# Kernel optimization log

Measured on AMD Instinct MI355X. Metric: run time of the kernel, lower is better.

The kernel has to match this reference:

```python
import jax, jax.numpy as jnp
import numpy as np

IN_DIM, H1, H2, N_CLASSES = 128, 100, 128, 19
BATCH, SEQ = 512, 256


def _lstm_relu(x, W, U, b, units):
    """Keras LSTM with activation='relu', recurrent_activation='sigmoid'.
    x: [B, T, D]. Returns (all hidden states [B, T, units], last hidden [B, units]).
    Gate order (Keras): i, f, g(cell candidate), o.
    """
    B = x.shape[0]
    h0 = jnp.zeros((B, units), x.dtype)
    c0 = jnp.zeros((B, units), x.dtype)

    # precompute input projections for all timesteps: [T, B, 4*units]
    zx = jnp.einsum('btd,dk->tbk', x, W) + b

    def step(carry, zx_t):
        h, c = carry
        z = zx_t + h @ U
        i, f, g, o = jnp.split(z, 4, axis=-1)
        i = jax.nn.sigmoid(i)
        f = jax.nn.sigmoid(f)
        g = jax.nn.relu(g)          # activation='relu'
        o = jax.nn.sigmoid(o)
        c = f * c + i * g
        h = o * jax.nn.relu(c)      # output activation is also relu
        return (h, c), h

    (h_last, _), hs = jax.lax.scan(step, (h0, c0), zx)
    return jnp.transpose(hs, (1, 0, 2)), h_last


def setup_inputs() -> dict:
    key = jax.random.key(0)
    ks = jax.random.split(key, 9)
    def w(k, shape, fan_in):
        return jax.random.normal(k, shape, jnp.float32) / np.sqrt(fan_in)
    x = jax.random.normal(ks[0], (BATCH, SEQ, IN_DIM), jnp.float32)
    return {
        'x': x,
        'W1': w(ks[1], (IN_DIM, 4 * H1), IN_DIM),
        'U1': w(ks[2], (H1, 4 * H1), H1),
        'b1': jnp.zeros((4 * H1,), jnp.float32),
        'W2': w(ks[3], (H1, 4 * H2), H1),
        'U2': w(ks[4], (H2, 4 * H2), H2),
        'b2': jnp.zeros((4 * H2,), jnp.float32),
        'Wd': w(ks[5], (H2, N_CLASSES), H2),
        'bd': jnp.zeros((N_CLASSES,), jnp.float32),
    }


def reference(x, W1, U1, b1, W2, U2, b2, Wd, bd):
    h1_seq, _ = _lstm_relu(x, W1, U1, b1, H1)      # [B, T, 100]
    _, h2 = _lstm_relu(h1_seq, W2, U2, b2, H2)     # [B, 128] (last step only)
    logits = h2 @ Wd + bd
    return jax.nn.softmax(logits, axis=-1)         # [B, 19]
```

## Files before the change

kernel.cpp:

```cpp
#include <hip/hip_runtime.h>
#include <math.h>


#define T_SEQ 256
#define BATCH 512
#define IN_DIM 128
#define H1 100
#define H2 128
#define NCLS 19

typedef float f4v __attribute__((ext_vector_type(4)));

__device__ __forceinline__ float sigmoidf_(float x) {
    return 1.0f / (1.0f + __expf(-x));
}
__device__ __forceinline__ float hsum4_(f4v v) {
    return (v.x + v.y) + (v.z + v.w);
}

#define REP7(M)  M(0) M(1) M(2) M(3) M(4) M(5) M(6)
#define REP8(M)  M(0) M(1) M(2) M(3) M(4) M(5) M(6) M(7)

template<int K, int N, bool SWAP>
__global__ __launch_bounds__(256, 2)
void proj_kernel(const float* __restrict__ A, const float* __restrict__ W,
                 const float* __restrict__ bias, float* __restrict__ out)
{
    constexpr int LD = 132;
    __shared__ __align__(16) float As[32 * LD];
    __shared__ __align__(16) float Ws[32 * LD];
    const int tid = threadIdx.x;
    const int r0 = blockIdx.x * 128;
    const int c0 = blockIdx.y * 128;
    const int ty = tid >> 4, tx = tid & 15;

#define PACC(i) f4v accL##i = {0.f,0.f,0.f,0.f}; f4v accR##i = {0.f,0.f,0.f,0.f};
    REP8(PACC)
#undef PACC

    for (int kk = 0; kk < K; kk += 32) {
        __syncthreads();
#pragma unroll
        for (int i = 0; i < 4; ++i) {
            int idx = tid + i * 256;
            int row = idx >> 3, kg = idx & 7;
            int k = kk + kg * 4;
            f4v v = {0.f, 0.f, 0.f, 0.f};
            if (k < K) v = *(const f4v*)&A[(size_t)(r0 + row) * K + k];
            As[(kg * 4 + 0) * LD + row] = v.x;
            As[(kg * 4 + 1) * LD + row] = v.y;
            As[(kg * 4 + 2) * LD + row] = v.z;
            As[(kg * 4 + 3) * LD + row] = v.w;
        }
#pragma unroll
        for (int i = 0; i < 4; ++i) {
            int idx = tid + i * 256;
            int k = idx >> 5, cg = idx & 31;
            int gk = kk + k, gc = c0 + cg * 4;
            f4v v = {0.f, 0.f, 0.f, 0.f};
            if (gk < K && gc < N) v = *(const f4v*)&W[(size_t)gk * N + gc];
            *(f4v*)&Ws[k * LD + cg * 4] = v;
        }
        __syncthreads();
#pragma unroll
        for (int k = 0; k < 32; ++k) {
            f4v av0 = *(const f4v*)&As[k * LD + ty * 8];
            f4v av1 = *(const f4v*)&As[k * LD + ty * 8 + 4];
            f4v b0v = *(const f4v*)&Ws[k * LD + tx * 8];
            f4v b1v = *(const f4v*)&Ws[k * LD + tx * 8 + 4];
#define PFMA(i, s) accL##i += (s) * b0v; accR##i += (s) * b1v;
            PFMA(0, av0.x) PFMA(1, av0.y) PFMA(2, av0.z) PFMA(3, av0.w)
            PFMA(4, av1.x) PFMA(5, av1.y) PFMA(6, av1.z) PFMA(7, av1.w)
#undef PFMA
        }
    }

    const int cb = c0 + tx * 8;
    float b0 = (cb + 0 < N) ? bias[cb + 0] : 0.f;
    float b1 = (cb + 1 < N) ? bias[cb + 1] : 0.f;
    float b2 = (cb + 2 < N) ? bias[cb + 2] : 0.f;
    float b3 = (cb + 3 < N) ? bias[cb + 3] : 0.f;
    float b4 = (cb + 4 < N) ? bias[cb + 4] : 0.f;
    float b5 = (cb + 5 < N) ? bias[cb + 5] : 0.f;
    float b6 = (cb + 6 < N) ? bias[cb + 6] : 0.f;
    float b7 = (cb + 7 < N) ? bias[cb + 7] : 0.f;
    f4v bL = {b0, b1, b2, b3};
    f4v bR = {b4, b5, b6, b7};
#define PST(i) { \
        int r = r0 + ty * 8 + i; \
        size_t orow = SWAP ? ((size_t)(r & 255) * BATCH + (r >> 8)) : (size_t)r; \
        if (cb < N)     { f4v v = accL##i + bL; *(f4v*)&out[orow * N + cb] = v; } \
        if (cb + 4 < N) { f4v v = accR##i + bR; *(f4v*)&out[orow * N + cb + 4] = v; } }
    REP8(PST)
#undef PST
}

__device__ __forceinline__ f4v ldw_(const float* __restrict__ U1, int kb, int col) {
    f4v v;
    v.x = (kb + 0 < H1) ? U1[(size_t)(kb + 0) * 400 + col] : 0.f;
    v.y = (kb + 1 < H1) ? U1[(size_t)(kb + 1) * 400 + col] : 0.f;
    v.z = (kb + 2 < H1) ? U1[(size_t)(kb + 2) * 400 + col] : 0.f;
    v.w = (kb + 3 < H1) ? U1[(size_t)(kb + 3) * 400 + col] : 0.f;
    return v;
}

__global__ __launch_bounds__(512)
__attribute__((amdgpu_waves_per_eu(2, 2)))
void rec1_kernel(const float* __restrict__ zx,
                 const float* __restrict__ U1,
                 float* __restrict__ h1seq)
{
    const int row = blockIdx.x;
    const int tid = threadIdx.x;
    const int kq = tid >> 7;
    const int cl = tid & 127;
    const int cc = (cl < H1) ? cl : 0;
    __shared__ __align__(16) float hsP[112];
    __shared__ __align__(16) float zp[4][4][128];

#define R1W(j) \
    f4v w0_##j = ldw_(U1, kq * 28 + 4 * (j), cc); \
    f4v w1_##j = ldw_(U1, kq * 28 + 4 * (j), 100 + cc); \
    f4v w2_##j = ldw_(U1, kq * 28 + 4 * (j), 200 + cc); \
    f4v w3_##j = ldw_(U1, kq * 28 + 4 * (j), 300 + cc);
    REP7(R1W)
#undef R1W

    if (tid < 112) hsP[tid] = 0.0f;
    const bool tail = (kq == 0) && (cl < H1);
    float cst = 0.0f;
    float zc0 = 0.f, zc1 = 0.f, zc2 = 0.f, zc3 = 0.f;
    if (tail) {
        const float* pz = zx + (size_t)row * 400 + cl;
        zc0 = pz[0]; zc1 = pz[100]; zc2 = pz[200]; zc3 = pz[300];
    }
    __syncthreads();

    for (int t = 0; t < T_SEQ; ++t) {
        f4v s0 = {0.f, 0.f, 0.f, 0.f};
        f4v s1 = {0.f, 0.f, 0.f, 0.f};
        f4v s2 = {0.f, 0.f, 0.f, 0.f};
        f4v s3 = {0.f, 0.f, 0.f, 0.f};
#define R1F(j) { f4v hv = *(const f4v*)&hsP[kq * 28 + 4 * (j)]; \
        s0 += hv * w0_##j; s1 += hv * w1_##j; s2 += hv * w2_##j; s3 += hv * w3_##j; }
        REP7(R1F)
#undef R1F
        zp[kq][0][cl] = hsum4_(s0);
        zp[kq][1][cl] = hsum4_(s1);
        zp[kq][2][cl] = hsum4_(s2);
        zp[kq][3][cl] = hsum4_(s3);
        __syncthreads();

        if (tail) {
            int tn = (t + 1 < T_SEQ) ? t + 1 : t;
            const float* pz = zx + ((size_t)tn * BATCH + row) * 400 + cl;
            float zn0 = pz[0], zn1 = pz[100], zn2 = pz[200], zn3 = pz[300];

            float z0 = zc0 + ((zp[0][0][cl] + zp[1][0][cl]) + (zp[2][0][cl] + zp[3][0][cl]));
            float z1 = zc1 + ((zp[0][1][cl] + zp[1][1][cl]) + (zp[2][1][cl] + zp[3][1][cl]));
            float z2 = zc2 + ((zp[0][2][cl] + zp[1][2][cl]) + (zp[2][2][cl] + zp[3][2][cl]));
            float z3 = zc3 + ((zp[0][3][cl] + zp[1][3][cl]) + (zp[2][3][cl] + zp[3][3][cl]));
            float iv = sigmoidf_(z0);
            float fv = sigmoidf_(z1);
            float gv = fmaxf(z2, 0.0f);
            float ov = sigmoidf_(z3);
            cst = fv * cst + iv * gv;
            float h = ov * fmaxf(cst, 0.0f);
            hsP[cl] = h;
            h1seq[((size_t)t * BATCH + row) * H1 + cl] = h;
            zc0 = zn0; zc1 = zn1; zc2 = zn2; zc3 = zn3;
        }
        __syncthreads();
    }
}

template<bool INIT, bool LAST>
__global__ __launch_bounds__(512)
__attribute__((amdgpu_waves_per_eu(2, 2)))
void rec2_chunk(const float* __restrict__ zx,
                const float* __restrict__ U2,
                float* __restrict__ cbuf,
                float* __restrict__ hbuf,
                float* __restrict__ h2out,
                int tlen)
{
    const int row = blockIdx.x;
    const int tid = threadIdx.x;
    const int kq = tid >> 7;
    const int cl = tid & 127;
    __shared__ __align__(16) float hs[H2];
    __shared__ float zp[4 * 512];
    __shared__ float za[512];

#define R2_LD(j) \
    f4v w0_##j, w1_##j, w2_##j, w3_##j; { \
        const float* p = U2 + (size_t)(kq * 32 + 4 * j) * 512 + cl; \
        w0_##j = (f4v){p[0],   p[512],       p[1024],       p[1536]}; \
        w1_##j = (f4v){p[128], p[512 + 128], p[1024 + 128], p[1536 + 128]}; \
        w2_##j = (f4v){p[256], p[512 + 256], p[1024 + 256], p[1536 + 256]}; \
        w3_##j = (f4v){p[384], p[512 + 384], p[1024 + 384], p[1536 + 384]}; }
    REP8(R2_LD)
#undef R2_LD

    float cst = 0.0f;
    if (tid < H2) {
        if (INIT) {
            hs[tid] = 0.0f;
        } else {
            hs[tid] = hbuf[(size_t)row * H2 + tid];
            cst = cbuf[(size_t)row * H2 + tid];
        }
    }
    float zc = zx[(size_t)row * 512 + tid];
    __syncthreads();

    for (int t = 0; t < tlen; ++t) {
        int tn = (t + 1 < tlen) ? t + 1 : t;
        float zn = zx[((size_t)tn * BATCH + row) * 512 + tid];

        f4v s0 = {0.f, 0.f, 0.f, 0.f};
        f4v s1 = {0.f, 0.f, 0.f, 0.f};
        f4v s2 = {0.f, 0.f, 0.f, 0.f};
        f4v s3 = {0.f, 0.f, 0.f, 0.f};
#define R2_FMA(j) { f4v hv = *(const f4v*)&hs[kq * 32 + 4 * j]; \
        s0 += hv * w0_##j; s1 += hv * w1_##j; s2 += hv * w2_##j; s3 += hv * w3_##j; }
        REP8(R2_FMA)
#undef R2_FMA
        zp[kq * 512 + cl]       = hsum4_(s0);
        zp[kq * 512 + cl + 128] = hsum4_(s1);
        zp[kq * 512 + cl + 256] = hsum4_(s2);
        zp[kq * 512 + cl + 384] = hsum4_(s3);
        __syncthreads();

        float z = zc + (zp[tid] + zp[512 + tid]) + (zp[1024 + tid] + zp[1536 + tid]);
        float a = (tid >= 2 * H2 && tid < 3 * H2) ? fmaxf(z, 0.0f) : sigmoidf_(z);
        za[tid] = a;
        __syncthreads();

        if (tid < H2) {
            float i = za[tid], f = za[tid + 128], g = za[tid + 256], o = za[tid + 384];
            cst = f * cst + i * g;
            hs[tid] = o * fmaxf(cst, 0.0f);
        }
        __syncthreads();
        zc = zn;
    }

    if (tid < H2) {
        float h = hs[tid];
        cbuf[(size_t)row * H2 + tid] = cst;
        hbuf[(size_t)row * H2 + tid] = h;
        if (LAST) h2out[(size_t)row * H2 + tid] = h;
    }
}

__global__ __launch_bounds__(64, 1)
void dense_softmax_kernel(const float* __restrict__ h2, const float* __restrict__ Wd,
                          const float* __restrict__ bd, float* __restrict__ out)
{
    const int b = blockIdx.x;
    const int k = threadIdx.x;
    __shared__ __align__(16) float hsm[H2];
    if (k < H2 / 4) ((f4v*)hsm)[k] = ((const f4v*)(h2 + (size_t)b * H2))[k];
    __syncthreads();

    float logit = -1e30f;
    if (k < NCLS) {
        float acc = bd[k];
#pragma unroll
        for (int d = 0; d < H2; ++d) acc += hsm[d] * Wd[d * NCLS + k];
        logit = acc;
    }
    float m = logit;
#pragma unroll
    for (int off = 32; off >= 1; off >>= 1) m = fmaxf(m, __shfl_xor(m, off, 64));
    float e = (k < NCLS) ? __expf(logit - m) : 0.0f;
    float s = e;
#pragma unroll
    for (int off = 32; off >= 1; off >>= 1) s += __shfl_xor(s, off, 64);
    if (k < NCLS) out[(size_t)b * NCLS + k] = e / s;
}

__global__ __launch_bounds__(448, 1)
void lstm1_fb(const float* __restrict__ x, const float* __restrict__ W1,
              const float* __restrict__ U1, const float* __restrict__ b1,
              float* __restrict__ h1out)
{
    const int b = blockIdx.x;
    const int k = threadIdx.x;
    __shared__ __align__(16) float xs[IN_DIM];
    __shared__ __align__(16) float hs[H1];
    __shared__ __align__(16) float zs[4 * H1];
    float w1r[IN_DIM];
    float u1r[H1];
    float bias = 0.0f;
    if (k < 4 * H1) {
        bias = b1[k];
#pragma unroll
        for (int d = 0; d < IN_DIM; ++d) w1r[d] = W1[d * (4 * H1) + k];
#pragma unroll
        for (int j = 0; j < H1; ++j) u1r[j] = U1[j * (4 * H1) + k];
    }
    if (k < H1) hs[k] = 0.0f;
    if (k < IN_DIM / 4)
        ((float4*)xs)[k] = ((const float4*)(x + ((size_t)b * T_SEQ) * IN_DIM))[k];
    float c = 0.0f;
    __syncthreads();
    for (int t = 0; t < T_SEQ; ++t) {
        if (k < 4 * H1) {
            float acc0 = bias, acc1 = 0.f, acc2 = 0.f, acc3 = 0.f;
#pragma unroll
            for (int q = 0; q < IN_DIM / 4; ++q) {
                float4 xv = ((const float4*)xs)[q];
                acc0 += xv.x * w1r[4 * q]; acc1 += xv.y * w1r[4 * q + 1];
                acc2 += xv.z * w1r[4 * q + 2]; acc3 += xv.w * w1r[4 * q + 3];
            }
#pragma unroll
            for (int q = 0; q < H1 / 4; ++q) {
                float4 hv = ((const float4*)hs)[q];
                acc0 += hv.x * u1r[4 * q]; acc1 += hv.y * u1r[4 * q + 1];
                acc2 += hv.z * u1r[4 * q + 2]; acc3 += hv.w * u1r[4 * q + 3];
            }
            float zv = (acc0 + acc1) + (acc2 + acc3);
            zs[k] = (k >= 2 * H1 && k < 3 * H1) ? fmaxf(zv, 0.0f) : sigmoidf_(zv);
        }
        __syncthreads();
        if (k < H1) {
            float i = zs[k], f = zs[k + H1], g = zs[k + 2 * H1], o = zs[k + 3 * H1];
            c = f * c + i * g;
            float h = o * fmaxf(c, 0.0f);
            hs[k] = h;
            h1out[((size_t)t * BATCH + b) * H1 + k] = h;
        }
        int tn = t + 1;
        if (tn < T_SEQ && k < IN_DIM / 4)
            ((float4*)xs)[k] = ((const float4*)(x + ((size_t)b * T_SEQ + tn) * IN_DIM))[k];
        __syncthreads();
    }
}

__global__ __launch_bounds__(512, 1)
void lstm2_fb(const float* __restrict__ h1in, const float* __restrict__ W2,
              const float* __restrict__ U2, const float* __restrict__ b2,
              float* __restrict__ h2out)
{
    const int b = blockIdx.x;
    const int k = threadIdx.x;
    __shared__ __align__(16) float ps[H1];
    __shared__ __align__(16) float hs[H2];
    __shared__ __align__(16) float zs[4 * H2];
    float w2r[H1];
    float u2r[H2];
    float bias = b2[k];
#pragma unroll
    for (int j = 0; j < H1; ++j) w2r[j] = W2[j * (4 * H2) + k];
#pragma unroll
    for (int j = 0; j < H2; ++j) u2r[j] = U2[j * (4 * H2) + k];
    if (k < H2) hs[k] = 0.0f;
    if (k < H1 / 4)
        ((float4*)ps)[k] = ((const float4*)(h1in + (size_t)b * H1))[k];
    float c = 0.0f;
    float hlast = 0.0f;
    __syncthreads();
    for (int t = 0; t < T_SEQ; ++t) {
        float acc0 = bias, acc1 = 0.f, acc2 = 0.f, acc3 = 0.f;
#pragma unroll
        for (int q = 0; q < H1 / 4; ++q) {
            float4 pv = ((const float4*)ps)[q];
            acc0 += pv.x * w2r[4 * q]; acc1 += pv.y * w2r[4 * q + 1];
            acc2 += pv.z * w2r[4 * q + 2]; acc3 += pv.w * w2r[4 * q + 3];
        }
#pragma unroll
        for (int q = 0; q < H2 / 4; ++q) {
            float4 hv = ((const float4*)hs)[q];
            acc0 += hv.x * u2r[4 * q]; acc1 += hv.y * u2r[4 * q + 1];
            acc2 += hv.z * u2r[4 * q + 2]; acc3 += hv.w * u2r[4 * q + 3];
        }
        float zv = (acc0 + acc1) + (acc2 + acc3);
        zs[k] = (k >= 2 * H2 && k < 3 * H2) ? fmaxf(zv, 0.0f) : sigmoidf_(zv);
        __syncthreads();
        if (k < H2) {
            float i = zs[k], f = zs[k + H2], g = zs[k + 2 * H2], o = zs[k + 3 * H2];
            c = f * c + i * g;
            hlast = o * fmaxf(c, 0.0f);
            hs[k] = hlast;
        }
        int tn = t + 1;
        if (tn < T_SEQ && k < H1 / 4)
            ((float4*)ps)[k] = ((const float4*)(h1in + ((size_t)tn * BATCH + b) * H1))[k];
        __syncthreads();
    }
    if (k < H2) h2out[(size_t)b * H2 + k] = hlast;
}

extern "C" void kernel_launch(void* const* d_in, const int* in_sizes, int n_in,
                              void* d_out, int out_size, void* d_ws, size_t ws_size,
                              hipStream_t stream) {
    const float* x  = (const float*)d_in[0];
    const float* W1 = (const float*)d_in[1];
    const float* U1 = (const float*)d_in[2];
    const float* b1 = (const float*)d_in[3];
    const float* W2 = (const float*)d_in[4];
    const float* U2 = (const float*)d_in[5];
    const float* b2 = (const float*)d_in[6];
    const float* Wd = (const float*)d_in[7];
    const float* bd = (const float*)d_in[8];
    float* out = (float*)d_out;

    const size_t zx_elems = (size_t)T_SEQ * BATCH * 400;
    const size_t h1_elems = (size_t)T_SEQ * BATCH * H1;
    const size_t st_elems = (size_t)BATCH * H2;
    const size_t need = (zx_elems + h1_elems + 3 * st_elems) * sizeof(float);

    if (ws_size >= need) {
        float* zxbuf = (float*)d_ws;
        float* h1buf = zxbuf + zx_elems;
        float* cbuf  = h1buf + h1_elems;
        float* hbuf  = cbuf + st_elems;
        float* h2buf = hbuf + st_elems;
        const int TC = T_SEQ / 2;

        hipLaunchKernelGGL((proj_kernel<IN_DIM, 4 * H1, true>), dim3(1024, 4), dim3(256), 0, stream,
                           x, W1, b1, zxbuf);
        hipLaunchKernelGGL(rec1_kernel, dim3(BATCH), dim3(512), 0, stream,
                           zxbuf, U1, h1buf);
        hipLaunchKernelGGL((proj_kernel<H1, 4 * H2, false>), dim3(512, 4), dim3(256), 0, stream,
                           h1buf, W2, b2, zxbuf);
        hipLaunchKernelGGL((rec2_chunk<true, false>), dim3(BATCH), dim3(512), 0, stream,
                           zxbuf, U2, cbuf, hbuf, h2buf, TC);
        hipLaunchKernelGGL((proj_kernel<H1, 4 * H2, false>), dim3(512, 4), dim3(256), 0, stream,
                           h1buf + (size_t)TC * BATCH * H1, W2, b2, zxbuf);
        hipLaunchKernelGGL((rec2_chunk<false, true>), dim3(BATCH), dim3(512), 0, stream,
                           zxbuf, U2, cbuf, hbuf, h2buf, TC);

        hipLaunchKernelGGL(dense_softmax_kernel, dim3(BATCH), dim3(64), 0, stream,
                           h2buf, Wd, bd, out);
    } else {
        float* h1buf = (float*)d_ws;
        float* h2buf = h1buf + h1_elems;
        hipLaunchKernelGGL(lstm1_fb, dim3(BATCH), dim3(448), 0, stream, x, W1, U1, b1, h1buf);
        hipLaunchKernelGGL(lstm2_fb, dim3(BATCH), dim3(512), 0, stream, h1buf, W2, U2, b2, h2buf);
        hipLaunchKernelGGL(dense_softmax_kernel, dim3(BATCH), dim3(64), 0, stream, h2buf, Wd, bd, out);
    }
}
```

Measured before the change: 1.285 ms.

## Reduce layer-1 gate partials with quad shuffles and double-buffer hidden state

```diff
diff --git a/kernel.cpp b/kernel.cpp
--- a/kernel.cpp
+++ b/kernel.cpp
@@ -96,11 +96,15 @@
 }
 
 __device__ __forceinline__ f4v ldw_(const float* __restrict__ U1, int kb, int col) {
+    int k0 = (kb + 0 < H1) ? kb + 0 : H1 - 1;
+    int k1 = (kb + 1 < H1) ? kb + 1 : H1 - 1;
+    int k2 = (kb + 2 < H1) ? kb + 2 : H1 - 1;
+    int k3 = (kb + 3 < H1) ? kb + 3 : H1 - 1;
     f4v v;
-    v.x = (kb + 0 < H1) ? U1[(size_t)(kb + 0) * 400 + col] : 0.f;
-    v.y = (kb + 1 < H1) ? U1[(size_t)(kb + 1) * 400 + col] : 0.f;
-    v.z = (kb + 2 < H1) ? U1[(size_t)(kb + 2) * 400 + col] : 0.f;
-    v.w = (kb + 3 < H1) ? U1[(size_t)(kb + 3) * 400 + col] : 0.f;
+    v.x = U1[(size_t)k0 * 400 + col];
+    v.y = U1[(size_t)k1 * 400 + col];
+    v.z = U1[(size_t)k2 * 400 + col];
+    v.w = U1[(size_t)k3 * 400 + col];
     return v;
 }
 
@@ -112,11 +116,10 @@
 {
     const int row = blockIdx.x;
     const int tid = threadIdx.x;
-    const int kq = tid >> 7;
-    const int cl = tid & 127;
+    const int cl = tid >> 2;
+    const int kq = tid & 3;
     const int cc = (cl < H1) ? cl : 0;
-    __shared__ __align__(16) float hsP[112];
-    __shared__ __align__(16) float zp[4][4][128];
+    __shared__ __align__(16) float hsP[2][112];
 
 #define R1W(j) \
     f4v w0_##j = ldw_(U1, kq * 28 + 4 * (j), cc); \
@@ -126,7 +129,7 @@
     REP7(R1W)
 #undef R1W
 
-    if (tid < 112) hsP[tid] = 0.0f;
+    if (tid < 112) { hsP[0][tid] = 0.0f; hsP[1][tid] = 0.0f; }
     const bool tail = (kq == 0) && (cl < H1);
     float cst = 0.0f;
     float zc0 = 0.f, zc1 = 0.f, zc2 = 0.f, zc3 = 0.f;
@@ -137,36 +140,43 @@
     __syncthreads();
 
     for (int t = 0; t < T_SEQ; ++t) {
+        float zn0 = 0.f, zn1 = 0.f, zn2 = 0.f, zn3 = 0.f;
+        if (tail) {
+            int tn = (t + 1 < T_SEQ) ? t + 1 : t;
+            const float* pz = zx + ((size_t)tn * BATCH + row) * 400 + cl;
+            zn0 = pz[0]; zn1 = pz[100]; zn2 = pz[200]; zn3 = pz[300];
+        }
+
+        const float* hb = hsP[t & 1];
         f4v s0 = {0.f, 0.f, 0.f, 0.f};
         f4v s1 = {0.f, 0.f, 0.f, 0.f};
         f4v s2 = {0.f, 0.f, 0.f, 0.f};
         f4v s3 = {0.f, 0.f, 0.f, 0.f};
-#define R1F(j) { f4v hv = *(const f4v*)&hsP[kq * 28 + 4 * (j)]; \
+#define R1F(j) { f4v hv = *(const f4v*)&hb[kq * 28 + 4 * (j)]; \
         s0 += hv * w0_##j; s1 += hv * w1_##j; s2 += hv * w2_##j; s3 += hv * w3_##j; }
         REP7(R1F)
 #undef R1F
-        zp[kq][0][cl] = hsum4_(s0);
-        zp[kq][1][cl] = hsum4_(s1);
-        zp[kq][2][cl] = hsum4_(s2);
-        zp[kq][3][cl] = hsum4_(s3);
-        __syncthreads();
+        float a0 = hsum4_(s0);
+        float a1 = hsum4_(s1);
+        float a2 = hsum4_(s2);
+        float a3 = hsum4_(s3);
+        a0 += __shfl_xor(a0, 1, 64); a0 += __shfl_xor(a0, 2, 64);
+        a1 += __shfl_xor(a1, 1, 64); a1 += __shfl_xor(a1, 2, 64);
+        a2 += __shfl_xor(a2, 1, 64); a2 += __shfl_xor(a2, 2, 64);
+        a3 += __shfl_xor(a3, 1, 64); a3 += __shfl_xor(a3, 2, 64);
 
         if (tail) {
-            int tn = (t + 1 < T_SEQ) ? t + 1 : t;
-            const float* pz = zx + ((size_t)tn * BATCH + row) * 400 + cl;
-            float zn0 = pz[0], zn1 = pz[100], zn2 = pz[200], zn3 = pz[300];
-
-            float z0 = zc0 + ((zp[0][0][cl] + zp[1][0][cl]) + (zp[2][0][cl] + zp[3][0][cl]));
-            float z1 = zc1 + ((zp[0][1][cl] + zp[1][1][cl]) + (zp[2][1][cl] + zp[3][1][cl]));
-            float z2 = zc2 + ((zp[0][2][cl] + zp[1][2][cl]) + (zp[2][2][cl] + zp[3][2][cl]));
-            float z3 = zc3 + ((zp[0][3][cl] + zp[1][3][cl]) + (zp[2][3][cl] + zp[3][3][cl]));
+            float z0 = zc0 + a0;
+            float z1 = zc1 + a1;
+            float z2 = zc2 + a2;
+            float z3 = zc3 + a3;
             float iv = sigmoidf_(z0);
             float fv = sigmoidf_(z1);
             float gv = fmaxf(z2, 0.0f);
             float ov = sigmoidf_(z3);
             cst = fv * cst + iv * gv;
             float h = ov * fmaxf(cst, 0.0f);
-            hsP[cl] = h;
+            hsP[(t + 1) & 1][cl] = h;
             h1seq[((size_t)t * BATCH + row) * H1 + cl] = h;
             zc0 = zn0; zc1 = zn1; zc2 = zn2; zc3 = zn3;
         }
```

New measurement: 1.345 ms. +4.7%, slower.
